# Kernel tuning notes

Measured on AMD Instinct MI355X. Metric: run time of the kernel, lower is better.

Reference implementation:

```python
import jax, jax.numpy as jnp
import numpy as np

B, S, D = 2, 2048, 1024
H = 16
HD = D // H


def setup_inputs() -> dict:
    key = jax.random.key(0)
    ks = jax.random.split(key, 6)
    x = jax.random.normal(ks[0], (B, S, D), dtype=jnp.float32)
    scale = 1.0 / np.sqrt(D)
    Wq = jax.random.normal(ks[1], (D, D), dtype=jnp.float32) * scale
    Wk = jax.random.normal(ks[2], (D, D), dtype=jnp.float32) * scale
    Wv = jax.random.normal(ks[3], (D, D), dtype=jnp.float32) * scale
    Wo = jax.random.normal(ks[4], (D, D), dtype=jnp.float32) * scale
    bo = jax.random.normal(ks[5], (D,), dtype=jnp.float32) * 0.01
    return {"x": x, "Wq": Wq, "Wk": Wk, "Wv": Wv, "Wo": Wo, "bo": bo}


def reference(x, Wq, Wk, Wv, Wo, bo):
    b, t, _ = x.shape
    # QKV projections (no bias), split into heads: [b, h, t, hd]
    q = (x @ Wq).reshape(b, t, H, HD).transpose(0, 2, 1, 3)
    k = (x @ Wk).reshape(b, t, H, HD).transpose(0, 2, 1, 3)
    v = (x @ Wv).reshape(b, t, H, HD).transpose(0, 2, 1, 3)
    # scores [b, h, t, t]; causal mask (upper triangle -> -inf) applied before scaling
    scores = jnp.einsum("bhqd,bhkd->bhqk", q, k)
    causal = jnp.triu(jnp.ones((t, t), dtype=bool), k=1)
    scores = jnp.where(causal, -jnp.inf, scores)
    attn = jax.nn.softmax(scores / jnp.sqrt(jnp.asarray(HD, scores.dtype)), axis=-1)
    ctx = jnp.einsum("bhqk,bhkd->bhqd", attn, v)
    ctx = ctx.transpose(0, 2, 1, 3).reshape(b, t, H * HD)
    return ctx @ Wo + bo
```

## Files before the change

kernel.cpp:

```cpp
#include <hip/hip_runtime.h>

#define B_ 2
#define S_ 2048
#define D_ 1024
#define H_ 16
#define HD_ 64
#define M_ (B_*S_)

typedef __attribute__((ext_vector_type(8))) short bf16x8;
typedef __attribute__((ext_vector_type(4))) short s16x4;
typedef __attribute__((ext_vector_type(4))) float f32x4;
typedef __attribute__((ext_vector_type(4))) unsigned int u32x4;

static __device__ __forceinline__ unsigned short f2bf(float f) {
  unsigned int u = __builtin_bit_cast(unsigned int, f);
  u += 0x7FFFu + ((u >> 16) & 1u);
  return (unsigned short)(u >> 16);
}

static __device__ __forceinline__ unsigned int cvt_pk_bf16(float a, float b) {
  unsigned int r;
  asm("v_cvt_pk_bf16_f32 %0, %1, %2" : "=v"(r) : "v"(a), "v"(b));
  return r;
}

static __device__ __forceinline__ void gload_lds16(const void* g, void* l) {
  __builtin_amdgcn_global_load_lds(
      (const __attribute__((address_space(1))) unsigned int*)g,
      (__attribute__((address_space(3))) unsigned int*)l, 16, 0, 0);
}

__global__ __launch_bounds__(256) void xcvt_kernel(const float* __restrict__ x,
                                                   unsigned short* __restrict__ xb) {
  size_t i = ((size_t)blockIdx.x * 256 + threadIdx.x) * 8;
  float4 a = ((const float4*)(x + i))[0];
  float4 b = ((const float4*)(x + i))[1];
  bf16x8 w;
  w[0]=(short)f2bf(a.x); w[1]=(short)f2bf(a.y); w[2]=(short)f2bf(a.z); w[3]=(short)f2bf(a.w);
  w[4]=(short)f2bf(b.x); w[5]=(short)f2bf(b.y); w[6]=(short)f2bf(b.z); w[7]=(short)f2bf(b.w);
  *(bf16x8*)(xb + i) = w;
}

__global__ void wtrans_kernel(const float* __restrict__ Wq, const float* __restrict__ Wk,
                              const float* __restrict__ Wv, const float* __restrict__ Wo,
                              unsigned short* __restrict__ wt) {
  __shared__ float tile[32][33];
  const float* W = blockIdx.z==0 ? Wq : blockIdx.z==1 ? Wk : blockIdx.z==2 ? Wv : Wo;
  unsigned short* out = wt + (size_t)blockIdx.z * D_ * D_;
  int n0 = blockIdx.x*32, k0 = blockIdx.y*32;
  int tx = threadIdx.x, ty = threadIdx.y;
  #pragma unroll
  for (int i=0;i<4;i++) tile[ty+i*8][tx] = W[(size_t)(k0+ty+i*8)*D_ + n0+tx];
  __syncthreads();
  #pragma unroll
  for (int i=0;i<4;i++) out[(size_t)(n0+ty+i*8)*D_ + (k0+tx)] = f2bf(tile[tx][ty+i*8]);
}

#define GEMM_K_LOOP(Abase, Bbase)                                                     \
  for (int ks = 0; ks < 16; ++ks) {                                                   \
    const int k0 = ks * 64;                                                           \
    __syncthreads();                                                                  \
    _Pragma("unroll")                                                                 \
    for (int p = 0; p < 4; ++p) {                                                     \
      int c = p*256 + t;                                                              \
      int row = c >> 3, sl = (c & 7) ^ (row & 7);                                     \
      gload_lds16(Abase + (size_t)row*D_ + k0 + sl*8, &As[(p*256 + wid*64)*8]);       \
    }                                                                                 \
    _Pragma("unroll")                                                                 \
    for (int p = 0; p < 4; ++p) {                                                     \
      int c = p*256 + t;                                                              \
      int row = c >> 3, sl = (c & 7) ^ (row & 7);                                     \
      gload_lds16(Bbase + (size_t)row*D_ + k0 + sl*8, &Bs[(p*256 + wid*64)*8]);       \
    }                                                                                 \
    __syncthreads();                                                                  \
    _Pragma("unroll")                                                                 \
    for (int kk = 0; kk < 2; ++kk) {                                                  \
      bf16x8 af[4], bfr[4];                                                           \
      _Pragma("unroll")                                                               \
      for (int m = 0; m < 4; ++m) {                                                   \
        int row = wr + m*16 + l15;                                                    \
        af[m] = *(const bf16x8*)((const char*)As + row*128 + (((kk*4+lg)^(row&7))<<4)); \
      }                                                                               \
      _Pragma("unroll")                                                               \
      for (int n = 0; n < 4; ++n) {                                                   \
        int row = wc + n*16 + l15;                                                    \
        bfr[n] = *(const bf16x8*)((const char*)Bs + row*128 + (((kk*4+lg)^(row&7))<<4)); \
      }                                                                               \
      _Pragma("unroll")                                                               \
      for (int m = 0; m < 4; ++m)                                                     \
        _Pragma("unroll")                                                             \
        for (int n = 0; n < 4; ++n)                                                   \
          acc[m][n] = __builtin_amdgcn_mfma_f32_16x16x32_bf16(af[m], bfr[n], acc[m][n], 0,0,0); \
    }                                                                                 \
  }

__global__ __launch_bounds__(256,3) void gemm_qkv_kernel(
    const unsigned short* __restrict__ xb, const unsigned short* __restrict__ wt,
    unsigned short* __restrict__ Qo, unsigned short* __restrict__ Ko,
    unsigned short* __restrict__ Vto) {
  __shared__ __align__(16) unsigned short As[128*64];
  __shared__ __align__(16) unsigned short Bs[128*64];
  const int z = blockIdx.z;
  const int m0 = blockIdx.y*128, n0 = blockIdx.x*128;
  const int t = threadIdx.x, lane = t & 63, wid = t >> 6;
  const int wr = (wid>>1)*64, wc = (wid&1)*64;
  const int l15 = lane & 15, lg = lane >> 4;
  const unsigned short* Ab = xb + (size_t)m0 * D_;
  const unsigned short* Bb = wt + (size_t)z * D_ * D_ + (size_t)n0 * D_;

  f32x4 acc[4][4];
  #pragma unroll
  for (int m=0;m<4;m++)
    #pragma unroll
    for (int n=0;n<4;n++) acc[m][n] = f32x4{0.f,0.f,0.f,0.f};

  GEMM_K_LOOP(Ab, Bb)

  const float qscale = 0.18033688011112042f;
  #pragma unroll
  for (int m=0;m<4;m++) {
    #pragma unroll
    for (int n=0;n<4;n++) {
      #pragma unroll
      for (int r=0;r<4;r++) {
        int gm = m0 + wr + m*16 + lg*4 + r;
        int gn = n0 + wc + n*16 + l15;
        int b = gm >> 11, s = gm & (S_-1);
        int h = gn >> 6,  d = gn & 63;
        float av = acc[m][n][r];
        if (z==0) av *= qscale;
        unsigned short val = f2bf(av);
        if (z==0)      Qo[(((size_t)(b*H_+h))*S_ + s)*HD_ + d] = val;
        else if (z==1) Ko[(((size_t)(b*H_+h))*S_ + s)*HD_ + d] = val;
        else           Vto[(((size_t)(b*H_+h))*HD_ + d)*S_ + s] = val;
      }
    }
  }
}

__global__ __launch_bounds__(256,3) void attn_kernel(
    const unsigned short* __restrict__ Q, const unsigned short* __restrict__ K,
    const unsigned short* __restrict__ Vt, unsigned short* __restrict__ ctx) {
  __shared__ __align__(16) unsigned short KT[2][64*64];
  __shared__ __align__(16) unsigned short VT[2][64*64];
  __shared__ __align__(16) unsigned short PL[4][16*72];
  const int t = threadIdx.x, lane = t & 63, wid = t >> 6;
  const int bh = blockIdx.x & 31;
  const int qt = 31 - (int)(blockIdx.x >> 5);
  const int b = bh >> 4, h = bh & 15;
  const int q0 = qt * 64, qw0 = q0 + wid * 16;
  const int nchunk = qt + 1;
  const unsigned short* Qp = Q  + (size_t)bh * S_ * HD_;
  const unsigned short* Kp = K  + (size_t)bh * S_ * HD_;
  const unsigned short* Vp = Vt + (size_t)bh * HD_ * S_;
  const int l15 = lane & 15, lg = lane >> 4;
  const int rsub = lane >> 3, slot = lane & 7;
  const int sslot = slot ^ rsub;

  bf16x8 qf0 = *(const bf16x8*)(Qp + (size_t)(qw0 + l15)*HD_ + lg*8);
  bf16x8 qf1 = *(const bf16x8*)(Qp + (size_t)(qw0 + l15)*HD_ + 32 + lg*8);

  f32x4 o[4];
  #pragma unroll
  for (int dt=0;dt<4;dt++) o[dt] = f32x4{0.f,0.f,0.f,0.f};
  float lsum = 0.f;

  auto stage = [&](int ch, int buf) {
    const int kk0 = ch * 64;
    #pragma unroll
    for (int j=0;j<2;j++) {
      int row = 16*wid + 8*j + rsub;
      gload_lds16(Kp + (size_t)(kk0 + row)*HD_ + sslot*8, &KT[buf][(16*wid + 8*j)*64]);
      gload_lds16(Vp + (size_t)row*S_ + kk0 + sslot*8,    &VT[buf][(16*wid + 8*j)*64]);
    }
  };

  stage(0, 0);
  __syncthreads();

  for (int ch=0; ch<nchunk; ++ch) {
    const int cur = ch & 1;
    const int kk0 = ch * 64;
    if (ch + 1 < nchunk) stage(ch+1, cur^1);

    const unsigned short* Kt = &KT[cur][0];
    const unsigned short* Vv = &VT[cur][0];

    f32x4 st[4];
    #pragma unroll
    for (int kt=0; kt<4; ++kt) {
      int row = kt*16 + l15;
      int sw = (row & 7) << 4;
      bf16x8 kf0 = *(const bf16x8*)((const char*)Kt + row*128 + ((lg*16)      ^ sw));
      bf16x8 kf1 = *(const bf16x8*)((const char*)Kt + row*128 + ((64 + lg*16) ^ sw));
      f32x4 z = f32x4{0.f,0.f,0.f,0.f};
      z = __builtin_amdgcn_mfma_f32_16x16x32_bf16(kf0, qf0, z, 0,0,0);
      z = __builtin_amdgcn_mfma_f32_16x16x32_bf16(kf1, qf1, z, 0,0,0);
      st[kt] = z;
    }

    if (ch == nchunk-1) {
      const int q = qw0 + l15;
      #pragma unroll
      for (int kt=0;kt<4;kt++)
        #pragma unroll
        for (int r=0;r<4;r++)
          if (kk0 + kt*16 + lg*4 + r > q) st[kt][r] = -INFINITY;
    }

    float rs = 0.f;
    #pragma unroll
    for (int kt=0;kt<4;kt++) {
      #pragma unroll
      for (int r=0;r<4;r++) {
        float p = exp2f(st[kt][r]);
        st[kt][r] = p;
        rs += p;
      }
      uint2 pk;
      pk.x = cvt_pk_bf16(st[kt][0], st[kt][1]);
      pk.y = cvt_pk_bf16(st[kt][2], st[kt][3]);
      *(uint2*)&PL[wid][l15*72 + kt*16 + lg*4] = pk;
    }
    rs += __shfl_xor(rs, 16);
    rs += __shfl_xor(rs, 32);
    lsum += rs;

    bf16x8 pf0 = *(const bf16x8*)&PL[wid][l15*72 + lg*8];
    bf16x8 pf1 = *(const bf16x8*)&PL[wid][l15*72 + 32 + lg*8];

    #pragma unroll
    for (int dt=0;dt<4;dt++) {
      int row = dt*16 + l15;
      int sw = (row & 7) << 4;
      bf16x8 vf0 = *(const bf16x8*)((const char*)Vv + row*128 + ((lg*16)      ^ sw));
      bf16x8 vf1 = *(const bf16x8*)((const char*)Vv + row*128 + ((64 + lg*16) ^ sw));
      o[dt] = __builtin_amdgcn_mfma_f32_16x16x32_bf16(pf0, vf0, o[dt], 0,0,0);
      o[dt] = __builtin_amdgcn_mfma_f32_16x16x32_bf16(pf1, vf1, o[dt], 0,0,0);
    }

    __syncthreads();
  }

  float li = 1.f / lsum;
  float lr[4];
  #pragma unroll
  for (int r=0;r<4;r++) lr[r] = __shfl(li, lg*4 + r);
  #pragma unroll
  for (int dt=0;dt<4;dt++)
    #pragma unroll
    for (int r=0;r<4;r++) {
      size_t row = (size_t)(b*S_ + qw0 + lg*4 + r);
      ctx[row*D_ + h*HD_ + dt*16 + l15] = f2bf(o[dt][r] * lr[r]);
    }
}

__global__ __launch_bounds__(256,3) void gemm_out_kernel(
    const unsigned short* __restrict__ ctx, const unsigned short* __restrict__ WtO,
    const float* __restrict__ bo, float* __restrict__ out) {
  __shared__ __align__(16) unsigned short As[128*64];
  __shared__ __align__(16) unsigned short Bs[128*64];
  const int m0 = blockIdx.y*128, n0 = blockIdx.x*128;
  const int t = threadIdx.x, lane = t & 63, wid = t >> 6;
  const int wr = (wid>>1)*64, wc = (wid&1)*64;
  const int l15 = lane & 15, lg = lane >> 4;
  const unsigned short* Ab = ctx + (size_t)m0 * D_;
  const unsigned short* Bb = WtO + (size_t)n0 * D_;

  f32x4 acc[4][4];
  #pragma unroll
  for (int m=0;m<4;m++)
    #pragma unroll
    for (int n=0;n<4;n++) acc[m][n] = f32x4{0.f,0.f,0.f,0.f};

  GEMM_K_LOOP(Ab, Bb)

  #pragma unroll
  for (int n=0;n<4;n++) {
    float bias = bo[n0 + wc + n*16 + l15];
    #pragma unroll
    for (int m=0;m<4;m++)
      #pragma unroll
      for (int r=0;r<4;r++) {
        int gm = m0 + wr + m*16 + lg*4 + r;
        int gn = n0 + wc + n*16 + l15;
        out[(size_t)gm*D_ + gn] = acc[m][n][r] + bias;
      }
  }
}

extern "C" void kernel_launch(void* const* d_in, const int* in_sizes, int n_in,
                              void* d_out, int out_size, void* d_ws, size_t ws_size,
                              hipStream_t stream) {
  (void)in_sizes; (void)n_in; (void)out_size; (void)ws_size;
  const float* x  = (const float*)d_in[0];
  const float* Wq = (const float*)d_in[1];
  const float* Wk = (const float*)d_in[2];
  const float* Wv = (const float*)d_in[3];
  const float* Wo = (const float*)d_in[4];
  const float* bo = (const float*)d_in[5];
  float* out = (float*)d_out;

  unsigned short* wt  = (unsigned short*)d_ws;
  unsigned short* Qb  = wt  + (size_t)4*D_*D_;
  unsigned short* Kb  = Qb  + (size_t)M_*D_;
  unsigned short* Vtb = Kb  + (size_t)M_*D_;
  unsigned short* ctb = Vtb + (size_t)M_*D_;
  unsigned short* xbb = ctb + (size_t)M_*D_;

  xcvt_kernel<<<dim3(M_*D_/(256*8)), 256, 0, stream>>>(x, xbb);
  wtrans_kernel<<<dim3(32,32,4), dim3(32,8), 0, stream>>>(Wq, Wk, Wv, Wo, wt);
  gemm_qkv_kernel<<<dim3(8,32,3), 256, 0, stream>>>(xbb, wt, Qb, Kb, Vtb);
  attn_kernel<<<dim3(1024), 256, 0, stream>>>(Qb, Kb, Vtb, ctb);
  gemm_out_kernel<<<dim3(8,32), 256, 0, stream>>>(ctb, wt + (size_t)3*D_*D_, bo, out);
}
```

Measured before the change: 112.2 us.

## Switch attention to 32x32 MFMA tiles with register-resident P via permlane swap

The attention kernel now uses 2 waves per block, each handling 32 query rows with 32x32x16 bf16 MFMAs instead of 16x16x32. The softmax probabilities are repacked into A-operand layout in registers using v_permlane32_swap, which removes the per-wave LDS staging buffer for P and its round-trip. The goal is fewer LDS operations and better MFMA efficiency per K/V tile loaded. In exchange, each block has half the threads, accumulators use more registers, and K/V staging work per thread doubles.

```diff
diff --git a/kernel.cpp b/kernel.cpp
--- a/kernel.cpp
+++ b/kernel.cpp
@@ -10,6 +10,7 @@
 typedef __attribute__((ext_vector_type(8))) short bf16x8;
 typedef __attribute__((ext_vector_type(4))) short s16x4;
 typedef __attribute__((ext_vector_type(4))) float f32x4;
+typedef __attribute__((ext_vector_type(16))) float f32x16;
 typedef __attribute__((ext_vector_type(4))) unsigned int u32x4;
 
 static __device__ __forceinline__ unsigned short f2bf(float f) {
@@ -138,40 +139,42 @@
   }
 }
 
-__global__ __launch_bounds__(256,3) void attn_kernel(
+__global__ __launch_bounds__(128,2) void attn_kernel(
     const unsigned short* __restrict__ Q, const unsigned short* __restrict__ K,
     const unsigned short* __restrict__ Vt, unsigned short* __restrict__ ctx) {
   __shared__ __align__(16) unsigned short KT[2][64*64];
   __shared__ __align__(16) unsigned short VT[2][64*64];
-  __shared__ __align__(16) unsigned short PL[4][16*72];
   const int t = threadIdx.x, lane = t & 63, wid = t >> 6;
   const int bh = blockIdx.x & 31;
   const int qt = 31 - (int)(blockIdx.x >> 5);
   const int b = bh >> 4, h = bh & 15;
-  const int q0 = qt * 64, qw0 = q0 + wid * 16;
+  const int q0 = qt * 64, qw0 = q0 + wid * 32;
   const int nchunk = qt + 1;
   const unsigned short* Qp = Q  + (size_t)bh * S_ * HD_;
   const unsigned short* Kp = K  + (size_t)bh * S_ * HD_;
   const unsigned short* Vp = Vt + (size_t)bh * HD_ * S_;
-  const int l15 = lane & 15, lg = lane >> 4;
+  const int l31 = lane & 31, lh = lane >> 5;
   const int rsub = lane >> 3, slot = lane & 7;
   const int sslot = slot ^ rsub;
-
-  bf16x8 qf0 = *(const bf16x8*)(Qp + (size_t)(qw0 + l15)*HD_ + lg*8);
-  bf16x8 qf1 = *(const bf16x8*)(Qp + (size_t)(qw0 + l15)*HD_ + 32 + lg*8);
-
-  f32x4 o[4];
-  #pragma unroll
-  for (int dt=0;dt<4;dt++) o[dt] = f32x4{0.f,0.f,0.f,0.f};
+  const int swr = (l31 & 7) << 4;
+
+  bf16x8 qf[4];
+  #pragma unroll
+  for (int ds=0; ds<4; ++ds)
+    qf[ds] = *(const bf16x8*)(Qp + (size_t)(qw0 + l31)*HD_ + ds*16 + lh*8);
+
+  f32x16 o0, o1;
+  #pragma unroll
+  for (int i=0;i<16;i++) { o0[i]=0.f; o1[i]=0.f; }
   float lsum = 0.f;
 
   auto stage = [&](int ch, int buf) {
     const int kk0 = ch * 64;
     #pragma unroll
-    for (int j=0;j<2;j++) {
-      int row = 16*wid + 8*j + rsub;
-      gload_lds16(Kp + (size_t)(kk0 + row)*HD_ + sslot*8, &KT[buf][(16*wid + 8*j)*64]);
-      gload_lds16(Vp + (size_t)row*S_ + kk0 + sslot*8,    &VT[buf][(16*wid + 8*j)*64]);
+    for (int j=0;j<4;j++) {
+      int row = wid*32 + j*8 + rsub;
+      gload_lds16(Kp + (size_t)(kk0 + row)*HD_ + sslot*8, &KT[buf][(wid*32 + j*8)*64]);
+      gload_lds16(Vp + (size_t)row*S_ + kk0 + sslot*8,    &VT[buf][(wid*32 + j*8)*64]);
     }
   };
 
@@ -183,76 +186,87 @@
     const int kk0 = ch * 64;
     if (ch + 1 < nchunk) stage(ch+1, cur^1);
 
-    const unsigned short* Kt = &KT[cur][0];
-    const unsigned short* Vv = &VT[cur][0];
-
-    f32x4 st[4];
-    #pragma unroll
-    for (int kt=0; kt<4; ++kt) {
-      int row = kt*16 + l15;
-      int sw = (row & 7) << 4;
-      bf16x8 kf0 = *(const bf16x8*)((const char*)Kt + row*128 + ((lg*16)      ^ sw));
-      bf16x8 kf1 = *(const bf16x8*)((const char*)Kt + row*128 + ((64 + lg*16) ^ sw));
-      f32x4 z = f32x4{0.f,0.f,0.f,0.f};
-      z = __builtin_amdgcn_mfma_f32_16x16x32_bf16(kf0, qf0, z, 0,0,0);
-      z = __builtin_amdgcn_mfma_f32_16x16x32_bf16(kf1, qf1, z, 0,0,0);
-      st[kt] = z;
+    const char* Kt = (const char*)&KT[cur][0];
+    const char* Vv = (const char*)&VT[cur][0];
+
+    f32x16 s0, s1;
+    #pragma unroll
+    for (int i=0;i<16;i++) { s0[i]=0.f; s1[i]=0.f; }
+    #pragma unroll
+    for (int ds=0; ds<4; ++ds) {
+      bf16x8 kf0 = *(const bf16x8*)(Kt + l31*128        + ((ds*32 + lh*16) ^ swr));
+      bf16x8 kf1 = *(const bf16x8*)(Kt + (32+l31)*128   + ((ds*32 + lh*16) ^ swr));
+      s0 = __builtin_amdgcn_mfma_f32_32x32x16_bf16(kf0, qf[ds], s0, 0,0,0);
+      s1 = __builtin_amdgcn_mfma_f32_32x32x16_bf16(kf1, qf[ds], s1, 0,0,0);
     }
 
     if (ch == nchunk-1) {
-      const int q = qw0 + l15;
+      const int q = qw0 + l31;
       #pragma unroll
-      for (int kt=0;kt<4;kt++)
-        #pragma unroll
-        for (int r=0;r<4;r++)
-          if (kk0 + kt*16 + lg*4 + r > q) st[kt][r] = -INFINITY;
+      for (int r=0;r<16;r++) {
+        int kb = kk0 + (r&3) + 8*(r>>2) + 4*lh;
+        if (kb > q)      s0[r] = -INFINITY;
+        if (kb + 32 > q) s1[r] = -INFINITY;
+      }
     }
 
     float rs = 0.f;
     #pragma unroll
-    for (int kt=0;kt<4;kt++) {
-      #pragma unroll
-      for (int r=0;r<4;r++) {
-        float p = exp2f(st[kt][r]);
-        st[kt][r] = p;
-        rs += p;
-      }
-      uint2 pk;
-      pk.x = cvt_pk_bf16(st[kt][0], st[kt][1]);
-      pk.y = cvt_pk_bf16(st[kt][2], st[kt][3]);
-      *(uint2*)&PL[wid][l15*72 + kt*16 + lg*4] = pk;
-    }
-    rs += __shfl_xor(rs, 16);
+    for (int r=0;r<16;r++) {
+      float p0 = exp2f(s0[r]); s0[r] = p0; rs += p0;
+      float p1 = exp2f(s1[r]); s1[r] = p1; rs += p1;
+    }
     rs += __shfl_xor(rs, 32);
     lsum += rs;
 
-    bf16x8 pf0 = *(const bf16x8*)&PL[wid][l15*72 + lg*8];
-    bf16x8 pf1 = *(const bf16x8*)&PL[wid][l15*72 + 32 + lg*8];
-
-    #pragma unroll
-    for (int dt=0;dt<4;dt++) {
-      int row = dt*16 + l15;
-      int sw = (row & 7) << 4;
-      bf16x8 vf0 = *(const bf16x8*)((const char*)Vv + row*128 + ((lg*16)      ^ sw));
-      bf16x8 vf1 = *(const bf16x8*)((const char*)Vv + row*128 + ((64 + lg*16) ^ sw));
-      o[dt] = __builtin_amdgcn_mfma_f32_16x16x32_bf16(pf0, vf0, o[dt], 0,0,0);
-      o[dt] = __builtin_amdgcn_mfma_f32_16x16x32_bf16(pf1, vf1, o[dt], 0,0,0);
+    bf16x8 pa00, pa01, pa10, pa11;
+    #define MAKE_PA(SS, KS, OUT) {                                          \
+      unsigned int x0 = cvt_pk_bf16(SS[(KS)*8+0], SS[(KS)*8+1]);            \
+      unsigned int y0 = cvt_pk_bf16(SS[(KS)*8+4], SS[(KS)*8+5]);            \
+      unsigned int x1 = cvt_pk_bf16(SS[(KS)*8+2], SS[(KS)*8+3]);            \
+      unsigned int y1 = cvt_pk_bf16(SS[(KS)*8+6], SS[(KS)*8+7]);            \
+      asm volatile("v_permlane32_swap_b32 %0, %1" : "+v"(x0), "+v"(y0));    \
+      asm volatile("v_permlane32_swap_b32 %0, %1" : "+v"(x1), "+v"(y1));    \
+      u32x4 u; u[0]=x0; u[1]=x1; u[2]=y0; u[3]=y1;                          \
+      OUT = __builtin_bit_cast(bf16x8, u); }
+    MAKE_PA(s0, 0, pa00) MAKE_PA(s0, 1, pa01)
+    MAKE_PA(s1, 0, pa10) MAKE_PA(s1, 1, pa11)
+    #undef MAKE_PA
+
+    {
+      const char* v0r = Vv + l31*128;
+      const char* v1r = Vv + (32+l31)*128;
+      bf16x8 v;
+      v = *(const bf16x8*)(v0r + ((      lh*16) ^ swr));
+      o0 = __builtin_amdgcn_mfma_f32_32x32x16_bf16(pa00, v, o0, 0,0,0);
+      v = *(const bf16x8*)(v0r + ((32  + lh*16) ^ swr));
+      o0 = __builtin_amdgcn_mfma_f32_32x32x16_bf16(pa01, v, o0, 0,0,0);
+      v = *(const bf16x8*)(v0r + ((64  + lh*16) ^ swr));
+      o0 = __builtin_amdgcn_mfma_f32_32x32x16_bf16(pa10, v, o0, 0,0,0);
+      v = *(const bf16x8*)(v0r + ((96  + lh*16) ^ swr));
+      o0 = __builtin_amdgcn_mfma_f32_32x32x16_bf16(pa11, v, o0, 0,0,0);
+      v = *(const bf16x8*)(v1r + ((      lh*16) ^ swr));
+      o1 = __builtin_amdgcn_mfma_f32_32x32x16_bf16(pa00, v, o1, 0,0,0);
+      v = *(const bf16x8*)(v1r + ((32  + lh*16) ^ swr));
+      o1 = __builtin_amdgcn_mfma_f32_32x32x16_bf16(pa01, v, o1, 0,0,0);
+      v = *(const bf16x8*)(v1r + ((64  + lh*16) ^ swr));
+      o1 = __builtin_amdgcn_mfma_f32_32x32x16_bf16(pa10, v, o1, 0,0,0);
+      v = *(const bf16x8*)(v1r + ((96  + lh*16) ^ swr));
+      o1 = __builtin_amdgcn_mfma_f32_32x32x16_bf16(pa11, v, o1, 0,0,0);
     }
 
     __syncthreads();
   }
 
   float li = 1.f / lsum;
-  float lr[4];
-  #pragma unroll
-  for (int r=0;r<4;r++) lr[r] = __shfl(li, lg*4 + r);
-  #pragma unroll
-  for (int dt=0;dt<4;dt++)
-    #pragma unroll
-    for (int r=0;r<4;r++) {
-      size_t row = (size_t)(b*S_ + qw0 + lg*4 + r);
-      ctx[row*D_ + h*HD_ + dt*16 + l15] = f2bf(o[dt][r] * lr[r]);
-    }
+  #pragma unroll
+  for (int r=0;r<16;r++) {
+    int qloc = (r&3) + 8*(r>>2) + 4*lh;
+    float lr = __shfl(li, qloc);
+    size_t row = (size_t)(b*S_ + qw0 + qloc);
+    ctx[row*D_ + h*HD_ +      l31] = f2bf(o0[r] * lr);
+    ctx[row*D_ + h*HD_ + 32 + l31] = f2bf(o1[r] * lr);
+  }
 }
 
 __global__ __launch_bounds__(256,3) void gemm_out_kernel(
@@ -311,6 +325,6 @@
   xcvt_kernel<<<dim3(M_*D_/(256*8)), 256, 0, stream>>>(x, xbb);
   wtrans_kernel<<<dim3(32,32,4), dim3(32,8), 0, stream>>>(Wq, Wk, Wv, Wo, wt);
   gemm_qkv_kernel<<<dim3(8,32,3), 256, 0, stream>>>(xbb, wt, Qb, Kb, Vtb);
-  attn_kernel<<<dim3(1024), 256, 0, stream>>>(Qb, Kb, Vtb, ctb);
+  attn_kernel<<<dim3(1024), 128, 0, stream>>>(Qb, Kb, Vtb, ctb);
   gemm_out_kernel<<<dim3(8,32), 256, 0, stream>>>(ctb, wt + (size_t)3*D_*D_, bo, out);
 }
```

Measured after the change: 123.0 us. 1.1x slower.
